# Kernel tuning notes

Hardware: AMD Instinct MI355X
Metric: run time of the kernel (lower is better)

## Reference

```python
import jax, jax.numpy as jnp
import numpy as np

B, S, HID = 1, 4096, 2048
H, KVH, D = 8, 4, 256
SW = 1024          # sliding window
EPS = 1e-6
NEG = -1e30


def _rmsnorm(x, w=None, eps=EPS):
    # torch nn.RMSNorm: x / sqrt(mean(x^2) + eps) * weight
    y = x * jax.lax.rsqrt(jnp.mean(x * x, axis=-1, keepdims=True) + eps)
    return y * w if w is not None else y


def _rotate_half(x):
    x1, x2 = jnp.split(x, 2, axis=-1)
    return jnp.concatenate([-x2, x1], axis=-1)


def _rope(x, cos, sin):
    # x: [B,S,H,D]; cos/sin: [B,S,rot] -> [B,S,1,rot]; rot == D here (no pass-through)
    c = cos[:, :, None, :]
    s = sin[:, :, None, :]
    return x * c + _rotate_half(x) * s


def setup_inputs() -> dict:
    key = jax.random.key(0)
    ks = jax.random.split(key, 9)
    return {
        "hidden_states": jax.random.normal(ks[0], (B, S, HID), jnp.float32),
        "cos": jax.random.uniform(ks[1], (B, S, D), jnp.float32),
        "sin": jax.random.uniform(ks[2], (B, S, D), jnp.float32),
        "q_w": jax.random.normal(ks[3], (H * D, HID), jnp.float32) * 0.02,
        "k_w": jax.random.normal(ks[4], (KVH * D, HID), jnp.float32) * 0.02,
        "v_w": jax.random.normal(ks[5], (KVH * D, HID), jnp.float32) * 0.02,
        "o_w": jax.random.normal(ks[6], (HID, H * D), jnp.float32) * 0.02,
        "q_norm_w": jnp.ones((D,), jnp.float32),
        "k_norm_w": jnp.ones((D,), jnp.float32),
    }


def reference(hidden_states, cos, sin, q_w, k_w, v_w, o_w, q_norm_w, k_norm_w):
    b, s, _ = hidden_states.shape
    # Projections (no bias), reshape to [B,S,heads,D]
    q = (hidden_states @ q_w.T).reshape(b, s, H, D)
    k = (hidden_states @ k_w.T).reshape(b, s, KVH, D)
    v = (hidden_states @ v_w.T).reshape(b, s, KVH, D)
    # per-head RMSNorm (v_norm has no affine), then RoPE on q/k
    q = _rope(_rmsnorm(q, q_norm_w), cos, sin)
    k = _rope(_rmsnorm(k, k_norm_w), cos, sin)
    v = _rmsnorm(v)
    # flatten(0,1): packed tokens T = B*S
    T = b * s
    q = q.reshape(T, H, D).transpose(1, 0, 2)          # [H,T,D]
    k = k.reshape(T, KVH, D).transpose(1, 0, 2)        # [KVH,T,D]
    v = v.reshape(T, KVH, D).transpose(1, 0, 2)
    # GQA: repeat_interleave kv heads
    rep = H // KVH
    k = jnp.repeat(k, rep, axis=0)                     # [H,T,D]
    v = jnp.repeat(v, rep, axis=0)
    # causal + sliding-window mask (allowed: i-SW < j <= i), scale=1.0
    i = jnp.arange(T)[:, None]
    j = jnp.arange(T)[None, :]
    allowed = (j <= i) & ((i - j) < SW)                # [T,T] bool
    scores = jnp.einsum("htd,hsd->hts", q, k)          # [H,T,T]
    scores = jnp.where(allowed[None], scores, NEG)
    p = jax.nn.softmax(scores, axis=-1)
    out = jnp.einsum("hts,hsd->htd", p, v)             # [H,T,D]
    out = out.transpose(1, 0, 2).reshape(b, s, H * D)
    return out @ o_w.T
```

## Files before the change

### kernel.cpp

```cpp
#include <hip/hip_runtime.h>
#include <stdint.h>

typedef __bf16 bf16x8 __attribute__((ext_vector_type(8)));
typedef __bf16 bf16x4 __attribute__((ext_vector_type(4)));
typedef _Float16 f16x8 __attribute__((ext_vector_type(8)));
typedef _Float16 f16x4 __attribute__((ext_vector_type(4)));
typedef float f32x4v __attribute__((ext_vector_type(4)));

__device__ __forceinline__ void async_copy16(const void* gptr, void* ldsptr) {
  __builtin_amdgcn_global_load_lds(
      (const __attribute__((address_space(1))) void*)gptr,
      (__attribute__((address_space(3))) void*)ldsptr,
      16, 0, 0);
}

__global__ __launch_bounds__(256) void cvt_split(
    const float* __restrict__ src, __bf16* __restrict__ hi,
    __bf16* __restrict__ lo, int n4) {
  const int i = blockIdx.x * 256 + threadIdx.x;
  if (i < n4) {
    const float4 v = ((const float4*)src)[i];
    float vv[4] = {v.x, v.y, v.z, v.w};
    bf16x4 h, l;
    for (int j = 0; j < 4; ++j) {
      h[j] = (__bf16)vv[j];
      l[j] = (__bf16)(vv[j] - (float)h[j]);
    }
    ((bf16x4*)hi)[i] = h;
    ((bf16x4*)lo)[i] = l;
  }
}

__global__ __launch_bounds__(256) void cvt_split_f16(
    const float* __restrict__ src, _Float16* __restrict__ hi,
    _Float16* __restrict__ lo, int n4) {
  const int i = blockIdx.x * 256 + threadIdx.x;
  if (i < n4) {
    const float4 v = ((const float4*)src)[i];
    float vv[4] = {v.x, v.y, v.z, v.w};
    f16x4 h, l;
    for (int j = 0; j < 4; ++j) {
      h[j] = (_Float16)vv[j];
      l[j] = (_Float16)(vv[j] - (float)h[j]);
    }
    ((f16x4*)hi)[i] = h;
    ((f16x4*)lo)[i] = l;
  }
}

__global__ __launch_bounds__(256) void cvt_f16(
    const float* __restrict__ src, _Float16* __restrict__ hi, int n4) {
  const int i = blockIdx.x * 256 + threadIdx.x;
  if (i < n4) {
    const float4 v = ((const float4*)src)[i];
    f16x4 h = {(_Float16)v.x, (_Float16)v.y, (_Float16)v.z, (_Float16)v.w};
    ((f16x4*)hi)[i] = h;
  }
}

__global__ __launch_bounds__(256, 4) void gemm_qkv(
    const _Float16* __restrict__ Ah, const _Float16* __restrict__ Al,
    const _Float16* __restrict__ Bh, float* __restrict__ C) {
  const int K = 2048, ldc = 4096;
  __shared__ __align__(16) _Float16 Ash[128 * 32];
  __shared__ __align__(16) _Float16 Asl[128 * 32];
  __shared__ __align__(16) _Float16 Bsh[128 * 32];
  const int bid = blockIdx.x;
  const int xcd = bid & 7, c = bid >> 3;
  const int m0 = (c >> 2) * 128, n0 = (xcd * 4 + (c & 3)) * 128;
  const int tid = threadIdx.x;
  const int wid = tid >> 6, lane = tid & 63, l15 = lane & 15, quad = lane >> 4;
  const int wm = wid >> 1, wn = wid & 1;

  f32x4v acc[4][4] = {};

  for (int kb = 0; kb < K; kb += 32) {
    for (int it = 0; it < 2; ++it) {
      const int cc = (wid * 2 + it) * 64 + lane;
      const int row = cc >> 2;
      const int sc = (cc & 3) ^ ((row >> 1) & 3);
      const size_t ao = (size_t)(m0 + row) * K + kb + sc * 8;
      const size_t bo = (size_t)(n0 + row) * K + kb + sc * 8;
      const int dst = (wid * 2 + it) * 512;
      async_copy16(Ah + ao, &Ash[dst]);
      async_copy16(Al + ao, &Asl[dst]);
      async_copy16(Bh + bo, &Bsh[dst]);
    }
    __syncthreads();
    f16x8 afh[4], afl[4], bfh[4];
    for (int mt = 0; mt < 4; ++mt) {
      const int r = wm * 64 + mt * 16 + l15;
      const int o = r * 32 + ((quad ^ ((r >> 1) & 3)) * 8);
      afh[mt] = *(const f16x8*)&Ash[o];
      afl[mt] = *(const f16x8*)&Asl[o];
    }
    for (int nt = 0; nt < 4; ++nt) {
      const int r = wn * 64 + nt * 16 + l15;
      const int o = r * 32 + ((quad ^ ((r >> 1) & 3)) * 8);
      bfh[nt] = *(const f16x8*)&Bsh[o];
    }
    for (int mt = 0; mt < 4; ++mt)
      for (int nt = 0; nt < 4; ++nt) {
        acc[mt][nt] = __builtin_amdgcn_mfma_f32_16x16x32_f16(afh[mt], bfh[nt], acc[mt][nt], 0, 0, 0);
        acc[mt][nt] = __builtin_amdgcn_mfma_f32_16x16x32_f16(afl[mt], bfh[nt], acc[mt][nt], 0, 0, 0);
      }
    __syncthreads();
  }
  for (int mt = 0; mt < 4; ++mt)
    for (int nt = 0; nt < 4; ++nt) {
      const int row = m0 + wm * 64 + mt * 16 + quad * 4;
      const int col = n0 + wn * 64 + nt * 16 + l15;
      for (int r = 0; r < 4; ++r)
        C[(size_t)(row + r) * ldc + col] = acc[mt][nt][r];
    }
}

__global__ __launch_bounds__(64) void norm_rope(
    const float* __restrict__ qkv, const float* __restrict__ cosb,
    const float* __restrict__ sinb, const float* __restrict__ qnw,
    const float* __restrict__ knw,
    __bf16* __restrict__ qh, __bf16* __restrict__ ql,
    __bf16* __restrict__ kh, __bf16* __restrict__ kl,
    __bf16* __restrict__ vT) {
  const int s = blockIdx.x, c = blockIdx.y, lane = threadIdx.x;
  const int d0 = lane * 4;
  const float4 xv = *(const float4*)(qkv + (size_t)s * 4096 + c * 256 + d0);
  float v[4] = {xv.x, xv.y, xv.z, xv.w};
  float ss = v[0] * v[0] + v[1] * v[1] + v[2] * v[2] + v[3] * v[3];
  for (int off = 1; off < 64; off <<= 1) ss += __shfl_xor(ss, off);
  const float rn = rsqrtf(ss * (1.0f / 256.0f) + 1e-6f);
  if (c < 12) {
    const float* w = (c < 8) ? qnw : knw;
    float y[4], yp[4];
    for (int j = 0; j < 4; ++j) y[j] = v[j] * rn * w[d0 + j];
    for (int j = 0; j < 4; ++j) yp[j] = __shfl_xor(y[j], 32);
    for (int j = 0; j < 4; ++j) {
      const int d = d0 + j;
      const float rot = (d < 128) ? -yp[j] : yp[j];
      y[j] = y[j] * cosb[s * 256 + d] + rot * sinb[s * 256 + d];
    }
    const size_t o = (c < 8) ? ((size_t)c * 4096 + s) * 256 + d0
                             : ((size_t)(c - 8) * 4096 + s) * 256 + d0;
    __bf16* dh = (c < 8) ? qh : kh;
    __bf16* dl = (c < 8) ? ql : kl;
    bf16x4 hv, lv;
    for (int j = 0; j < 4; ++j) {
      hv[j] = (__bf16)y[j];
      lv[j] = (__bf16)(y[j] - (float)hv[j]);
    }
    *(bf16x4*)(dh + o) = hv;
    *(bf16x4*)(dl + o) = lv;
  } else {
    const int kvh = c - 12;
    for (int j = 0; j < 4; ++j)
      vT[(size_t)(kvh * 256 + d0 + j) * 4096 + s] = (__bf16)(v[j] * rn);
  }
}

__global__ __launch_bounds__(512, 2) void attn_mfma(
    const __bf16* __restrict__ Qh_, const __bf16* __restrict__ Ql_,
    const __bf16* __restrict__ Kh_, const __bf16* __restrict__ Kl_,
    const __bf16* __restrict__ VT, __bf16* __restrict__ Aout) {
  const int S = 4096, D = 256;
  const int bid = blockIdx.y * 32 + blockIdx.x;
  const int swz = (bid & 7) * 32 + (bid >> 3);
  const int h = swz >> 5;
  const int q0 = (swz & 31) * 128;
  const int tid = threadIdx.x;
  const int wid = tid >> 6, lane = tid & 63, l15 = lane & 15, quad = lane >> 4;
  const int kv = h >> 1;

  __shared__ __align__(16) __bf16 Ksh[2][32 * 256];
  __shared__ __align__(16) __bf16 Ksl[2][32 * 256];
  __shared__ __align__(16) __bf16 Vs[2][256 * 32];
  __shared__ __align__(16) __bf16 P[8][16][32];

  const __bf16* Khh = Kh_ + (size_t)kv * S * D;
  const __bf16* Khl = Kl_ + (size_t)kv * S * D;
  const __bf16* Vh = VT + (size_t)kv * D * S;

  auto stage = [&](int buf, int kt) {
    for (int set = 0; set < 2; ++set) {
      const int n = set * 512 + wid * 64 + lane;
      const int row = n >> 5, c = n & 31;
      const int sc = c ^ (row & 7);
      const size_t go = (size_t)(kt + row) * D + sc * 8;
      const int dst = (set * 512 + wid * 64) * 8;
      async_copy16(Khh + go, &Ksh[buf][dst]);
      async_copy16(Khl + go, &Ksl[buf][dst]);
      const int dim = n >> 2, kc = n & 3;
      const size_t vo = (size_t)dim * S + kt + (kc ^ ((dim >> 1) & 3)) * 8;
      async_copy16(Vh + vo, &Vs[buf][dst]);
    }
  };

  bf16x8 qfh[8], qfl[8];
  {
    const size_t qoff =
        (size_t)h * S * D + (size_t)(q0 + wid * 16 + l15) * D + quad * 8;
    for (int ks = 0; ks < 8; ++ks) {
      qfh[ks] = *(const bf16x8*)(Qh_ + qoff + ks * 32);
      qfl[ks] = *(const bf16x8*)(Ql_ + qoff + ks * 32);
    }
  }

  f32x4v O[16] = {};
  float mrow[4] = {-1e30f, -1e30f, -1e30f, -1e30f};
  float lrow[4] = {0.f, 0.f, 0.f, 0.f};

  const int lo = (q0 >= 1024) ? (q0 - 1024) : 0;
  const int hi = q0 + 96;
  const int iqmin = q0 + wid * 16;
  const int iqmax = iqmin + 15;

  stage(0, lo);
  __syncthreads();
  int cur = 0;

  for (int kt = lo; kt <= hi; kt += 32) {
    if (kt + 32 <= hi) stage(cur ^ 1, kt + 32);
    const bool active = (kt <= iqmax) && (kt + 31 >= iqmin - 1023);
    if (active) {
      f32x4v sa[2] = {};
      for (int nt = 0; nt < 2; ++nt) {
        const int row = nt * 16 + l15;
        const int rxk = row & 7;
        for (int ks = 0; ks < 8; ++ks) {
          const int c = (ks * 4 + quad) ^ rxk;
          const bf16x8 kh8 = *(const bf16x8*)&Ksh[cur][row * 256 + c * 8];
          const bf16x8 kl8 = *(const bf16x8*)&Ksl[cur][row * 256 + c * 8];
          sa[nt] = __builtin_amdgcn_mfma_f32_16x16x32_bf16(qfh[ks], kh8, sa[nt], 0, 0, 0);
          sa[nt] = __builtin_amdgcn_mfma_f32_16x16x32_bf16(qfh[ks], kl8, sa[nt], 0, 0, 0);
          sa[nt] = __builtin_amdgcn_mfma_f32_16x16x32_bf16(qfl[ks], kh8, sa[nt], 0, 0, 0);
        }
      }
      float al[4];
      for (int r = 0; r < 4; ++r) {
        const int i = q0 + wid * 16 + quad * 4 + r;
        float mx = -1e30f;
        for (int nt = 0; nt < 2; ++nt) {
          const int j = kt + nt * 16 + l15;
          const float svv = ((j <= i) && (i - j < 1024)) ? sa[nt][r] : -1e30f;
          sa[nt][r] = svv;
          mx = fmaxf(mx, svv);
        }
        for (int off = 1; off < 16; off <<= 1) mx = fmaxf(mx, __shfl_xor(mx, off));
        const float mn = fmaxf(mrow[r], mx);
        al[r] = __expf(mrow[r] - mn);
        float ps = 0.f;
        const int prow = quad * 4 + r;
        const int px = (prow >> 1) & 3;
        for (int nt = 0; nt < 2; ++nt) {
          const float p = (mn <= -1e29f) ? 0.f : __expf(sa[nt][r] - mn);
          const int pc = (nt * 2 + (l15 >> 3)) ^ px;
          P[wid][prow][pc * 8 + (l15 & 7)] = (__bf16)p;
          ps += p;
        }
        for (int off = 1; off < 16; off <<= 1) ps += __shfl_xor(ps, off);
        lrow[r] = lrow[r] * al[r] + ps;
        mrow[r] = mn;
      }
      for (int nt2 = 0; nt2 < 16; ++nt2)
        for (int r = 0; r < 4; ++r) O[nt2][r] *= al[r];
      __asm__ volatile("s_waitcnt lgkmcnt(0)" ::: "memory");
      __builtin_amdgcn_sched_barrier(0);
      const int prx = (l15 >> 1) & 3;
      const bf16x8 pf = *(const bf16x8*)&P[wid][l15][(quad ^ prx) * 8];
      for (int nt2 = 0; nt2 < 16; ++nt2) {
        const int dim = nt2 * 16 + l15;
        const int vq = quad ^ ((dim >> 1) & 3);
        const bf16x8 vf = *(const bf16x8*)&Vs[cur][(dim * 4 + vq) * 8];
        O[nt2] = __builtin_amdgcn_mfma_f32_16x16x32_bf16(pf, vf, O[nt2], 0, 0, 0);
      }
    }
    __syncthreads();
    cur ^= 1;
  }
  for (int nt2 = 0; nt2 < 16; ++nt2)
    for (int r = 0; r < 4; ++r) {
      const float o = O[nt2][r] / lrow[r];
      Aout[(size_t)(q0 + wid * 16 + quad * 4 + r) * 2048 + h * 256 + nt2 * 16 + l15] = (__bf16)o;
    }
}

__global__ __launch_bounds__(256, 2) void gemm_out(
    const __bf16* __restrict__ A, const float* __restrict__ B,
    float* __restrict__ C) {
  const int K = 2048, ldc = 2048;
  __shared__ __align__(16) __bf16 As[128 * 32];
  __shared__ __align__(16) __bf16 Bs[128 * 32];
  const int m0 = blockIdx.y * 128, n0 = blockIdx.x * 128;
  const int tid = threadIdx.x;
  const int wid = tid >> 6, lane = tid & 63, l15 = lane & 15, quad = lane >> 4;
  const int wm = wid >> 1, wn = wid & 1;

  f32x4v acc[4][4] = {};

  for (int kb = 0; kb < K; kb += 32) {
    for (int cc = 0; cc < 2; ++cc) {
      const int c = cc * 256 + tid;
      const int row = c >> 2;
      const int col = ((c & 3) ^ ((row >> 1) & 3)) * 8;
      *(bf16x8*)&As[row * 32 + col] =
          *(const bf16x8*)(A + (size_t)(m0 + row) * K + kb + (c & 3) * 8);
    }
    for (int cc = 0; cc < 4; ++cc) {
      const int c = cc * 256 + tid;
      const int row = c >> 3;
      const int sl = ((c & 7) >> 1) ^ ((row >> 1) & 3);
      const int col = sl * 8 + (c & 1) * 4;
      const float4 bv = *(const float4*)(B + (size_t)(n0 + row) * K + kb + (c & 7) * 4);
      bf16x4 bh = {(__bf16)bv.x, (__bf16)bv.y, (__bf16)bv.z, (__bf16)bv.w};
      *(bf16x4*)&Bs[row * 32 + col] = bh;
    }
    __syncthreads();
    bf16x8 af[4], bfr[4];
    for (int mt = 0; mt < 4; ++mt) {
      const int r = wm * 64 + mt * 16 + l15;
      af[mt] = *(const bf16x8*)&As[r * 32 + ((quad ^ ((r >> 1) & 3)) * 8)];
    }
    for (int nt = 0; nt < 4; ++nt) {
      const int r = wn * 64 + nt * 16 + l15;
      bfr[nt] = *(const bf16x8*)&Bs[r * 32 + ((quad ^ ((r >> 1) & 3)) * 8)];
    }
    for (int mt = 0; mt < 4; ++mt)
      for (int nt = 0; nt < 4; ++nt)
        acc[mt][nt] = __builtin_amdgcn_mfma_f32_16x16x32_bf16(af[mt], bfr[nt], acc[mt][nt], 0, 0, 0);
    __syncthreads();
  }
  for (int mt = 0; mt < 4; ++mt)
    for (int nt = 0; nt < 4; ++nt) {
      const int row = m0 + wm * 64 + mt * 16 + quad * 4;
      const int col = n0 + wn * 64 + nt * 16 + l15;
      for (int r = 0; r < 4; ++r)
        C[(size_t)(row + r) * ldc + col] = acc[mt][nt][r];
    }
}

extern "C" void kernel_launch(void* const* d_in, const int* in_sizes, int n_in,
                              void* d_out, int out_size, void* d_ws, size_t ws_size,
                              hipStream_t stream) {
  const float* hidden = (const float*)d_in[0];
  const float* cosb   = (const float*)d_in[1];
  const float* sinb   = (const float*)d_in[2];
  const float* qw     = (const float*)d_in[3];
  const float* kw     = (const float*)d_in[4];
  const float* vw     = (const float*)d_in[5];
  const float* ow     = (const float*)d_in[6];
  const float* qnw    = (const float*)d_in[7];
  const float* knw    = (const float*)d_in[8];
  float* out = (float*)d_out;

  const size_t MB = 1048576;
  char* ws = (char*)d_ws;
  float*  qkvf = (float*)ws;
  __bf16* attn = (__bf16*)ws;
  _Float16* hh = (_Float16*)(ws + 64 * MB);
  _Float16* hl = (_Float16*)(ws + 80 * MB);
  _Float16* wh = (_Float16*)(ws + 96 * MB);
  __bf16* qh   = (__bf16*)(ws + 64 * MB);
  __bf16* ql   = (__bf16*)(ws + 80 * MB);
  __bf16* kh   = (__bf16*)(ws + 96 * MB);
  __bf16* kl   = (__bf16*)(ws + 104 * MB);
  __bf16* vT   = (__bf16*)(ws + 112 * MB);

  cvt_split_f16<<<dim3(8192), 256, 0, stream>>>(hidden, hh, hl, 2097152);
  cvt_f16<<<dim3(4096), 256, 0, stream>>>(qw, wh, 1048576);
  cvt_f16<<<dim3(2048), 256, 0, stream>>>(kw, wh + 4194304, 524288);
  cvt_f16<<<dim3(2048), 256, 0, stream>>>(vw, wh + 6291456, 524288);

  gemm_qkv<<<dim3(1024), 256, 0, stream>>>(hh, hl, wh, qkvf);
  norm_rope<<<dim3(4096, 16), 64, 0, stream>>>(qkvf, cosb, sinb, qnw, knw,
                                               qh, ql, kh, kl, vT);
  attn_mfma<<<dim3(32, 8), 512, 0, stream>>>(qh, ql, kh, kl, vT, attn);
  gemm_out<<<dim3(16, 32), 256, 0, stream>>>(attn, ow, out);
}
```

Before: 519.5 us.

## Switch attention and output GEMM to fp16, drop K low split

Attention tensors move from bf16 hi/lo splits to fp16. Q keeps its hi/lo split, but K keeps only the hi part, so QK^T needs two MFMAs per step instead of three and K-lo no longer has to be staged into LDS. The output projection now consumes a pre-converted fp16 weight through async global-to-LDS copies, with an XCD-aware block swizzle and a higher occupancy hint. An extra conversion kernel is added for o_w, and fp16 range or precision for the scores and P values is a possible accuracy risk.

```diff
diff --git a/kernel.cpp b/kernel.cpp
--- a/kernel.cpp
+++ b/kernel.cpp
@@ -12,23 +12,6 @@
       (const __attribute__((address_space(1))) void*)gptr,
       (__attribute__((address_space(3))) void*)ldsptr,
       16, 0, 0);
-}
-
-__global__ __launch_bounds__(256) void cvt_split(
-    const float* __restrict__ src, __bf16* __restrict__ hi,
-    __bf16* __restrict__ lo, int n4) {
-  const int i = blockIdx.x * 256 + threadIdx.x;
-  if (i < n4) {
-    const float4 v = ((const float4*)src)[i];
-    float vv[4] = {v.x, v.y, v.z, v.w};
-    bf16x4 h, l;
-    for (int j = 0; j < 4; ++j) {
-      h[j] = (__bf16)vv[j];
-      l[j] = (__bf16)(vv[j] - (float)h[j]);
-    }
-    ((bf16x4*)hi)[i] = h;
-    ((bf16x4*)lo)[i] = l;
-  }
 }
 
 __global__ __launch_bounds__(256) void cvt_split_f16(
@@ -119,9 +102,8 @@
     const float* __restrict__ qkv, const float* __restrict__ cosb,
     const float* __restrict__ sinb, const float* __restrict__ qnw,
     const float* __restrict__ knw,
-    __bf16* __restrict__ qh, __bf16* __restrict__ ql,
-    __bf16* __restrict__ kh, __bf16* __restrict__ kl,
-    __bf16* __restrict__ vT) {
+    _Float16* __restrict__ qh, _Float16* __restrict__ ql,
+    _Float16* __restrict__ kh, _Float16* __restrict__ vT) {
   const int s = blockIdx.x, c = blockIdx.y, lane = threadIdx.x;
   const int d0 = lane * 4;
   const float4 xv = *(const float4*)(qkv + (size_t)s * 4096 + c * 256 + d0);
@@ -139,28 +121,32 @@
       const float rot = (d < 128) ? -yp[j] : yp[j];
       y[j] = y[j] * cosb[s * 256 + d] + rot * sinb[s * 256 + d];
     }
-    const size_t o = (c < 8) ? ((size_t)c * 4096 + s) * 256 + d0
-                             : ((size_t)(c - 8) * 4096 + s) * 256 + d0;
-    __bf16* dh = (c < 8) ? qh : kh;
-    __bf16* dl = (c < 8) ? ql : kl;
-    bf16x4 hv, lv;
-    for (int j = 0; j < 4; ++j) {
-      hv[j] = (__bf16)y[j];
-      lv[j] = (__bf16)(y[j] - (float)hv[j]);
-    }
-    *(bf16x4*)(dh + o) = hv;
-    *(bf16x4*)(dl + o) = lv;
+    if (c < 8) {
+      const size_t o = ((size_t)c * 4096 + s) * 256 + d0;
+      f16x4 hv, lv;
+      for (int j = 0; j < 4; ++j) {
+        hv[j] = (_Float16)y[j];
+        lv[j] = (_Float16)(y[j] - (float)hv[j]);
+      }
+      *(f16x4*)(qh + o) = hv;
+      *(f16x4*)(ql + o) = lv;
+    } else {
+      const size_t o = ((size_t)(c - 8) * 4096 + s) * 256 + d0;
+      f16x4 hv;
+      for (int j = 0; j < 4; ++j) hv[j] = (_Float16)y[j];
+      *(f16x4*)(kh + o) = hv;
+    }
   } else {
     const int kvh = c - 12;
     for (int j = 0; j < 4; ++j)
-      vT[(size_t)(kvh * 256 + d0 + j) * 4096 + s] = (__bf16)(v[j] * rn);
+      vT[(size_t)(kvh * 256 + d0 + j) * 4096 + s] = (_Float16)(v[j] * rn);
   }
 }
 
 __global__ __launch_bounds__(512, 2) void attn_mfma(
-    const __bf16* __restrict__ Qh_, const __bf16* __restrict__ Ql_,
-    const __bf16* __restrict__ Kh_, const __bf16* __restrict__ Kl_,
-    const __bf16* __restrict__ VT, __bf16* __restrict__ Aout) {
+    const _Float16* __restrict__ Qh_, const _Float16* __restrict__ Ql_,
+    const _Float16* __restrict__ Kh_, const _Float16* __restrict__ VT,
+    _Float16* __restrict__ Aout) {
   const int S = 4096, D = 256;
   const int bid = blockIdx.y * 32 + blockIdx.x;
   const int swz = (bid & 7) * 32 + (bid >> 3);
@@ -170,14 +156,12 @@
   const int wid = tid >> 6, lane = tid & 63, l15 = lane & 15, quad = lane >> 4;
   const int kv = h >> 1;
 
-  __shared__ __align__(16) __bf16 Ksh[2][32 * 256];
-  __shared__ __align__(16) __bf16 Ksl[2][32 * 256];
-  __shared__ __align__(16) __bf16 Vs[2][256 * 32];
-  __shared__ __align__(16) __bf16 P[8][16][32];
-
-  const __bf16* Khh = Kh_ + (size_t)kv * S * D;
-  const __bf16* Khl = Kl_ + (size_t)kv * S * D;
-  const __bf16* Vh = VT + (size_t)kv * D * S;
+  __shared__ __align__(16) _Float16 Ksh[2][32 * 256];
+  __shared__ __align__(16) _Float16 Vs[2][256 * 32];
+  __shared__ __align__(16) _Float16 P[8][16][32];
+
+  const _Float16* Khh = Kh_ + (size_t)kv * S * D;
+  const _Float16* Vh = VT + (size_t)kv * D * S;
 
   auto stage = [&](int buf, int kt) {
     for (int set = 0; set < 2; ++set) {
@@ -187,20 +171,19 @@
       const size_t go = (size_t)(kt + row) * D + sc * 8;
       const int dst = (set * 512 + wid * 64) * 8;
       async_copy16(Khh + go, &Ksh[buf][dst]);
-      async_copy16(Khl + go, &Ksl[buf][dst]);
       const int dim = n >> 2, kc = n & 3;
       const size_t vo = (size_t)dim * S + kt + (kc ^ ((dim >> 1) & 3)) * 8;
       async_copy16(Vh + vo, &Vs[buf][dst]);
     }
   };
 
-  bf16x8 qfh[8], qfl[8];
+  f16x8 qfh[8], qfl[8];
   {
     const size_t qoff =
         (size_t)h * S * D + (size_t)(q0 + wid * 16 + l15) * D + quad * 8;
     for (int ks = 0; ks < 8; ++ks) {
-      qfh[ks] = *(const bf16x8*)(Qh_ + qoff + ks * 32);
-      qfl[ks] = *(const bf16x8*)(Ql_ + qoff + ks * 32);
+      qfh[ks] = *(const f16x8*)(Qh_ + qoff + ks * 32);
+      qfl[ks] = *(const f16x8*)(Ql_ + qoff + ks * 32);
     }
   }
 
@@ -227,11 +210,9 @@
         const int rxk = row & 7;
         for (int ks = 0; ks < 8; ++ks) {
           const int c = (ks * 4 + quad) ^ rxk;
-          const bf16x8 kh8 = *(const bf16x8*)&Ksh[cur][row * 256 + c * 8];
-          const bf16x8 kl8 = *(const bf16x8*)&Ksl[cur][row * 256 + c * 8];
-          sa[nt] = __builtin_amdgcn_mfma_f32_16x16x32_bf16(qfh[ks], kh8, sa[nt], 0, 0, 0);
-          sa[nt] = __builtin_amdgcn_mfma_f32_16x16x32_bf16(qfh[ks], kl8, sa[nt], 0, 0, 0);
-          sa[nt] = __builtin_amdgcn_mfma_f32_16x16x32_bf16(qfl[ks], kh8, sa[nt], 0, 0, 0);
+          const f16x8 kh8 = *(const f16x8*)&Ksh[cur][row * 256 + c * 8];
+          sa[nt] = __builtin_amdgcn_mfma_f32_16x16x32_f16(qfh[ks], kh8, sa[nt], 0, 0, 0);
+          sa[nt] = __builtin_amdgcn_mfma_f32_16x16x32_f16(qfl[ks], kh8, sa[nt], 0, 0, 0);
         }
       }
       float al[4];
@@ -253,7 +234,7 @@
         for (int nt = 0; nt < 2; ++nt) {
           const float p = (mn <= -1e29f) ? 0.f : __expf(sa[nt][r] - mn);
           const int pc = (nt * 2 + (l15 >> 3)) ^ px;
-          P[wid][prow][pc * 8 + (l15 & 7)] = (__bf16)p;
+          P[wid][prow][pc * 8 + (l15 & 7)] = (_Float16)p;
           ps += p;
         }
         for (int off = 1; off < 16; off <<= 1) ps += __shfl_xor(ps, off);
@@ -265,12 +246,12 @@
       __asm__ volatile("s_waitcnt lgkmcnt(0)" ::: "memory");
       __builtin_amdgcn_sched_barrier(0);
       const int prx = (l15 >> 1) & 3;
-      const bf16x8 pf = *(const bf16x8*)&P[wid][l15][(quad ^ prx) * 8];
+      const f16x8 pf = *(const f16x8*)&P[wid][l15][(quad ^ prx) * 8];
       for (int nt2 = 0; nt2 < 16; ++nt2) {
         const int dim = nt2 * 16 + l15;
         const int vq = quad ^ ((dim >> 1) & 3);
-        const bf16x8 vf = *(const bf16x8*)&Vs[cur][(dim * 4 + vq) * 8];
-        O[nt2] = __builtin_amdgcn_mfma_f32_16x16x32_bf16(pf, vf, O[nt2], 0, 0, 0);
+        const f16x8 vf = *(const f16x8*)&Vs[cur][(dim * 4 + vq) * 8];
+        O[nt2] = __builtin_amdgcn_mfma_f32_16x16x32_f16(pf, vf, O[nt2], 0, 0, 0);
       }
     }
     __syncthreads();
@@ -279,17 +260,19 @@
   for (int nt2 = 0; nt2 < 16; ++nt2)
     for (int r = 0; r < 4; ++r) {
       const float o = O[nt2][r] / lrow[r];
-      Aout[(size_t)(q0 + wid * 16 + quad * 4 + r) * 2048 + h * 256 + nt2 * 16 + l15] = (__bf16)o;
-    }
-}
-
-__global__ __launch_bounds__(256, 2) void gemm_out(
-    const __bf16* __restrict__ A, const float* __restrict__ B,
+      Aout[(size_t)(q0 + wid * 16 + quad * 4 + r) * 2048 + h * 256 + nt2 * 16 + l15] = (_Float16)o;
+    }
+}
+
+__global__ __launch_bounds__(256, 4) void gemm_out(
+    const _Float16* __restrict__ A, const _Float16* __restrict__ B,
     float* __restrict__ C) {
   const int K = 2048, ldc = 2048;
-  __shared__ __align__(16) __bf16 As[128 * 32];
-  __shared__ __align__(16) __bf16 Bs[128 * 32];
-  const int m0 = blockIdx.y * 128, n0 = blockIdx.x * 128;
+  __shared__ __align__(16) _Float16 As[128 * 32];
+  __shared__ __align__(16) _Float16 Bs[128 * 32];
+  const int bid = blockIdx.x;
+  const int xcd = bid & 7, c = bid >> 3;
+  const int m0 = (c >> 1) * 128, n0 = (xcd * 2 + (c & 1)) * 128;
   const int tid = threadIdx.x;
   const int wid = tid >> 6, lane = tid & 63, l15 = lane & 15, quad = lane >> 4;
   const int wm = wid >> 1, wn = wid & 1;
@@ -297,35 +280,29 @@
   f32x4v acc[4][4] = {};
 
   for (int kb = 0; kb < K; kb += 32) {
-    for (int cc = 0; cc < 2; ++cc) {
-      const int c = cc * 256 + tid;
-      const int row = c >> 2;
-      const int col = ((c & 3) ^ ((row >> 1) & 3)) * 8;
-      *(bf16x8*)&As[row * 32 + col] =
-          *(const bf16x8*)(A + (size_t)(m0 + row) * K + kb + (c & 3) * 8);
-    }
-    for (int cc = 0; cc < 4; ++cc) {
-      const int c = cc * 256 + tid;
-      const int row = c >> 3;
-      const int sl = ((c & 7) >> 1) ^ ((row >> 1) & 3);
-      const int col = sl * 8 + (c & 1) * 4;
-      const float4 bv = *(const float4*)(B + (size_t)(n0 + row) * K + kb + (c & 7) * 4);
-      bf16x4 bh = {(__bf16)bv.x, (__bf16)bv.y, (__bf16)bv.z, (__bf16)bv.w};
-      *(bf16x4*)&Bs[row * 32 + col] = bh;
-    }
-    __syncthreads();
-    bf16x8 af[4], bfr[4];
+    for (int it = 0; it < 2; ++it) {
+      const int cc = (wid * 2 + it) * 64 + lane;
+      const int row = cc >> 2;
+      const int sc = (cc & 3) ^ ((row >> 1) & 3);
+      const size_t ao = (size_t)(m0 + row) * K + kb + sc * 8;
+      const size_t bo = (size_t)(n0 + row) * K + kb + sc * 8;
+      const int dst = (wid * 2 + it) * 512;
+      async_copy16(A + ao, &As[dst]);
+      async_copy16(B + bo, &Bs[dst]);
+    }
+    __syncthreads();
+    f16x8 af[4], bfr[4];
     for (int mt = 0; mt < 4; ++mt) {
       const int r = wm * 64 + mt * 16 + l15;
-      af[mt] = *(const bf16x8*)&As[r * 32 + ((quad ^ ((r >> 1) & 3)) * 8)];
+      af[mt] = *(const f16x8*)&As[r * 32 + ((quad ^ ((r >> 1) & 3)) * 8)];
     }
     for (int nt = 0; nt < 4; ++nt) {
       const int r = wn * 64 + nt * 16 + l15;
-      bfr[nt] = *(const bf16x8*)&Bs[r * 32 + ((quad ^ ((r >> 1) & 3)) * 8)];
+      bfr[nt] = *(const f16x8*)&Bs[r * 32 + ((quad ^ ((r >> 1) & 3)) * 8)];
     }
     for (int mt = 0; mt < 4; ++mt)
       for (int nt = 0; nt < 4; ++nt)
-        acc[mt][nt] = __builtin_amdgcn_mfma_f32_16x16x32_bf16(af[mt], bfr[nt], acc[mt][nt], 0, 0, 0);
+        acc[mt][nt] = __builtin_amdgcn_mfma_f32_16x16x32_f16(af[mt], bfr[nt], acc[mt][nt], 0, 0, 0);
     __syncthreads();
   }
   for (int mt = 0; mt < 4; ++mt)
@@ -353,25 +330,26 @@
 
   const size_t MB = 1048576;
   char* ws = (char*)d_ws;
-  float*  qkvf = (float*)ws;
-  __bf16* attn = (__bf16*)ws;
-  _Float16* hh = (_Float16*)(ws + 64 * MB);
-  _Float16* hl = (_Float16*)(ws + 80 * MB);
-  _Float16* wh = (_Float16*)(ws + 96 * MB);
-  __bf16* qh   = (__bf16*)(ws + 64 * MB);
-  __bf16* ql   = (__bf16*)(ws + 80 * MB);
-  __bf16* kh   = (__bf16*)(ws + 96 * MB);
-  __bf16* kl   = (__bf16*)(ws + 104 * MB);
-  __bf16* vT   = (__bf16*)(ws + 112 * MB);
+  float*    qkvf = (float*)ws;
+  _Float16* attn = (_Float16*)ws;
+  _Float16* hh   = (_Float16*)(ws + 64 * MB);
+  _Float16* hl   = (_Float16*)(ws + 80 * MB);
+  _Float16* wh   = (_Float16*)(ws + 96 * MB);
+  _Float16* qh   = (_Float16*)(ws + 64 * MB);
+  _Float16* ql   = (_Float16*)(ws + 80 * MB);
+  _Float16* kh   = (_Float16*)(ws + 96 * MB);
+  _Float16* vT   = (_Float16*)(ws + 104 * MB);
+  _Float16* owh  = (_Float16*)(ws + 112 * MB);
 
   cvt_split_f16<<<dim3(8192), 256, 0, stream>>>(hidden, hh, hl, 2097152);
   cvt_f16<<<dim3(4096), 256, 0, stream>>>(qw, wh, 1048576);
   cvt_f16<<<dim3(2048), 256, 0, stream>>>(kw, wh + 4194304, 524288);
   cvt_f16<<<dim3(2048), 256, 0, stream>>>(vw, wh + 6291456, 524288);
+  cvt_f16<<<dim3(4096), 256, 0, stream>>>(ow, owh, 1048576);
 
   gemm_qkv<<<dim3(1024), 256, 0, stream>>>(hh, hl, wh, qkvf);
   norm_rope<<<dim3(4096, 16), 64, 0, stream>>>(qkvf, cosb, sinb, qnw, knw,
-                                               qh, ql, kh, kl, vT);
-  attn_mfma<<<dim3(32, 8), 512, 0, stream>>>(qh, ql, kh, kl, vT, attn);
-  gemm_out<<<dim3(16, 32), 256, 0, stream>>>(attn, ow, out);
-}
+                                               qh, ql, kh, vT);
+  attn_mfma<<<dim3(32, 8), 512, 0, stream>>>(qh, ql, kh, vT, attn);
+  gemm_out<<<dim3(512), 256, 0, stream>>>(attn, owh, out);
+}
```

Result: faster. 479.8 us (-7.7%).
